# Kernel tuning notes

Measured on AMD Instinct MI355X. Metric: run time of the kernel, lower is better.

Reference implementation:

```python
import jax, jax.numpy as jnp
import numpy as np

N_NODES = 50000
N_EDGES = 262144
HID = 256
N_CLS = 2


def setup_inputs() -> dict:
    key = jax.random.key(0)
    ks = jax.random.split(key, 6)
    node_repr = jax.random.normal(ks[0], (N_NODES, HID), dtype=jnp.float32)
    src = jax.random.randint(ks[1], (N_EDGES,), 0, N_NODES, dtype=jnp.int64)
    dst = jax.random.randint(ks[2], (N_EDGES,), 0, N_NODES, dtype=jnp.int64)
    # Linear weights stored as (in, out); init ~ torch default scale
    W1 = jax.random.normal(ks[3], (4 * HID, 2 * HID), dtype=jnp.float32) * (1.0 / np.sqrt(4 * HID))
    b1 = jnp.zeros((2 * HID,), dtype=jnp.float32)
    W2 = jax.random.normal(ks[4], (2 * HID, N_CLS), dtype=jnp.float32) * (1.0 / np.sqrt(2 * HID))
    b2 = jnp.zeros((N_CLS,), dtype=jnp.float32)
    return {"node_repr": node_repr, "src": src, "dst": dst,
            "W1": W1, "b1": b1, "W2": W2, "b2": b2}


def reference(node_repr, src, dst, W1, b1, W2, b2):
    h_i = node_repr[src]                      # [E, H] gather
    h_j = node_repr[dst]                      # [E, H] gather
    edge_input = jnp.concatenate(
        [h_i, h_j, jnp.abs(h_i - h_j), h_i * h_j], axis=1)  # [E, 4H]
    h = jax.nn.relu(edge_input @ W1 + b1)     # [E, 2H]; dropout = identity (eval)
    return h @ W2 + b2                        # [E, C]
```

## Files before the change

kernel.cpp:

```cpp
#include <hip/hip_runtime.h>

#define N_NODES 50000
#define E_EDGES 262144

typedef __attribute__((ext_vector_type(8))) short bf16x8;
typedef __attribute__((ext_vector_type(4))) float f32x4;

union V16 { uint4 u; bf16x8 h; };

__device__ __forceinline__ unsigned rne_pack(float a, float b) {
  unsigned ua = __float_as_uint(a); ua += 0x7fffu + ((ua >> 16) & 1u);
  unsigned ub = __float_as_uint(b); ub += 0x7fffu + ((ub >> 16) & 1u);
  return (ua >> 16) | (ub & 0xffff0000u);
}
__device__ __forceinline__ float bflo(unsigned u) { return __uint_as_float(u << 16); }
__device__ __forceinline__ float bfhi(unsigned u) { return __uint_as_float(u & 0xffff0000u); }
__device__ __forceinline__ unsigned perm_pack(float a, float b) {
  return __builtin_amdgcn_perm(__float_as_uint(b), __float_as_uint(a), 0x07060302u);
}
__device__ __forceinline__ void async_gather16(const void* gptr, void* lptr) {
  __builtin_amdgcn_global_load_lds(
      (const __attribute__((address_space(1))) void*)gptr,
      (__attribute__((address_space(3))) void*)lptr, 16, 0, 0);
}

__global__ void cvt_node_kernel(const float* __restrict__ x, unsigned short* __restrict__ y) {
  int i = (blockIdx.x * 256 + threadIdx.x) * 8;
  float4 f0 = *(const float4*)(x + i);
  float4 f1 = *(const float4*)(x + i + 4);
  uint4 o;
  o.x = rne_pack(f0.x, f0.y);
  o.y = rne_pack(f0.z, f0.w);
  o.z = rne_pack(f1.x, f1.y);
  o.w = rne_pack(f1.z, f1.w);
  *(uint4*)(y + i) = o;
}

__global__ void prep_w1pp2_kernel(const float* __restrict__ w1, unsigned short* __restrict__ w1pp2) {
  int t = blockIdx.x * 256 + threadIdx.x;
  int step = t >> 13;
  int rem = t & 8191;
  int sq = rem >> 9;
  int col = rem & 511;
  int s = sq >> 2, qd = sq & 3;
  int k0 = s * 256 + step * 32 + qd * 8;
  float f[8];
#pragma unroll
  for (int i = 0; i < 8; ++i) f[i] = w1[(size_t)(k0 + i) * 512 + col];
  uint4 o;
  o.x = rne_pack(f[0], f[1]);
  o.y = rne_pack(f[2], f[3]);
  o.z = rne_pack(f[4], f[5]);
  o.w = rne_pack(f[6], f[7]);
  *(uint4*)(w1pp2 + (size_t)t * 8) = o;
}

__global__ void init_out_kernel(float* __restrict__ out, const float* __restrict__ b2) {
  int i = blockIdx.x * 256 + threadIdx.x;
  float2 v; v.x = b2[0]; v.y = b2[1];
  *(float2*)(out + (size_t)i * 2) = v;
}

__global__ __launch_bounds__(256, 2) void edge_mlp_kernel(
    const unsigned short* __restrict__ nodeb,
    const unsigned short* __restrict__ w1pp2,
    const int* __restrict__ src,
    const int* __restrict__ dst,
    const float* __restrict__ b1,
    const float* __restrict__ w2,
    float* __restrict__ out) {
  __shared__ char smem[65536];

  const int tid = threadIdx.x;
  const int wid = tid >> 6;
  const int lane = tid & 63;
  const int quad = lane >> 4;
  const int l16 = lane & 15;
  const int bx = blockIdx.x;
  const int xc = bx & 7;
  const int t2 = bx >> 3;
  const int n_idx = t2 & 7;
  const int m_idx = (t2 >> 3) * 8 + xc;
  const int row0 = m_idx * 256;
  const int wrow0 = row0 + wid * 64;
  const int n0 = n_idx * 64;

  const char* nodeB = (const char*)nodeb;
  const char* w1B = (const char*)w1pp2;

  unsigned oi[4], oj[4];
#pragma unroll
  for (int c = 0; c < 4; ++c) {
    int e = (wid * 4 + c) * 16 + (lane >> 2);
    unsigned qg = (unsigned)(((lane & 3) ^ ((lane >> 3) & 3)) << 4);
    oi[c] = ((unsigned)src[row0 + e] << 9) + qg;
    oj[c] = ((unsigned)dst[row0 + e] << 9) + qg;
  }
  unsigned bOff[4];
#pragma unroll
  for (int s = 0; s < 4; ++s)
    bOff[s] = (unsigned)((s * 4 + quad) * 8192 + (n0 + l16) * 16);
  const char* w1s = w1B;

  const unsigned aR = (unsigned)((wid * 64 + l16) * 64 + ((quad ^ ((l16 >> 1) & 3)) << 4));

  f32x4 acc[4][4];
#pragma unroll
  for (int mt = 0; mt < 4; ++mt)
#pragma unroll
    for (int nt = 0; nt < 4; ++nt)
      acc[mt][nt] = (f32x4){0.f, 0.f, 0.f, 0.f};

#pragma unroll
  for (int c = 0; c < 4; ++c) {
    async_gather16(nodeB + oi[c], smem + (wid * 4 + c) * 1024);
    async_gather16(nodeB + oj[c], smem + 16384 + (wid * 4 + c) * 1024);
  }
  __syncthreads();

  int p = 0;
#pragma unroll 1
  for (int step = 0; step < 8; ++step) {
    const char* Acur = smem + (p << 15);
    V16 bf[4][4];
#pragma unroll
    for (int s = 0; s < 4; ++s)
#pragma unroll
      for (int nt = 0; nt < 4; ++nt)
        bf[s][nt].u = *(const uint4*)(w1s + bOff[s] + nt * 256);
    if (step < 7) {
      const unsigned aoN = (unsigned)(step + 1) * 64u;
      char* Aalt = smem + ((p ^ 1) << 15);
#pragma unroll
      for (int c = 0; c < 4; ++c) {
        async_gather16(nodeB + (oi[c] + aoN), Aalt + (wid * 4 + c) * 1024);
        async_gather16(nodeB + (oj[c] + aoN), Aalt + 16384 + (wid * 4 + c) * 1024);
      }
    }
    V16 hi[4], hj[4];
#pragma unroll
    for (int mt = 0; mt < 4; ++mt) {
      hi[mt].u = *(const uint4*)(Acur + aR + mt * 1024);
      hj[mt].u = *(const uint4*)(Acur + 16384 + aR + mt * 1024);
    }
#pragma unroll
    for (int sl = 0; sl < 2; ++sl) {
#pragma unroll
      for (int mt = 0; mt < 4; ++mt) {
        bf16x8 af = (sl == 0) ? hi[mt].h : hj[mt].h;
#pragma unroll
        for (int nt = 0; nt < 4; ++nt)
          acc[mt][nt] = __builtin_amdgcn_mfma_f32_16x16x32_bf16(af, bf[sl][nt].h, acc[mt][nt], 0, 0, 0);
      }
    }
#pragma unroll
    for (int mt = 0; mt < 4; ++mt) {
      const unsigned hw[4] = {hi[mt].u.x, hi[mt].u.y, hi[mt].u.z, hi[mt].u.w};
      const unsigned jw[4] = {hj[mt].u.x, hj[mt].u.y, hj[mt].u.z, hj[mt].u.w};
      unsigned d[4], pr[4];
#pragma unroll
      for (int w = 0; w < 4; ++w) {
        float i0 = bflo(hw[w]), i1 = bfhi(hw[w]);
        float j0 = bflo(jw[w]), j1 = bfhi(jw[w]);
        d[w] = perm_pack(i0 - j0, i1 - j1) & 0x7fff7fffu;
        pr[w] = perm_pack(i0 * j0, i1 * j1);
      }
      V16 a2, a3;
      a2.u = make_uint4(d[0], d[1], d[2], d[3]);
      a3.u = make_uint4(pr[0], pr[1], pr[2], pr[3]);
#pragma unroll
      for (int nt = 0; nt < 4; ++nt)
        acc[mt][nt] = __builtin_amdgcn_mfma_f32_16x16x32_bf16(a2.h, bf[2][nt].h, acc[mt][nt], 0, 0, 0);
#pragma unroll
      for (int nt = 0; nt < 4; ++nt)
        acc[mt][nt] = __builtin_amdgcn_mfma_f32_16x16x32_bf16(a3.h, bf[3][nt].h, acc[mt][nt], 0, 0, 0);
    }
    __syncthreads();
    w1s += 131072;
    p ^= 1;
  }

#pragma unroll
  for (int mt = 0; mt < 4; ++mt) {
    float pc0[4] = {0.f, 0.f, 0.f, 0.f};
    float pc1[4] = {0.f, 0.f, 0.f, 0.f};
#pragma unroll
    for (int nt = 0; nt < 4; ++nt) {
      int gc = n0 + nt * 16 + l16;
      float b1v = b1[gc];
      float w20 = w2[gc * 2 + 0];
      float w21 = w2[gc * 2 + 1];
#pragma unroll
      for (int r = 0; r < 4; ++r) {
        float v = fmaxf(acc[mt][nt][r] + b1v, 0.f);
        pc0[r] = fmaf(v, w20, pc0[r]);
        pc1[r] = fmaf(v, w21, pc1[r]);
      }
    }
#pragma unroll
    for (int r = 0; r < 4; ++r) {
      float s0 = pc0[r], s1 = pc1[r];
#pragma unroll
      for (int off = 1; off < 16; off <<= 1) {
        s0 += __shfl_xor(s0, off);
        s1 += __shfl_xor(s1, off);
      }
      int e = wrow0 + mt * 16 + quad * 4 + r;
      if (l16 == 0) unsafeAtomicAdd(&out[(size_t)e * 2 + 0], s0);
      if (l16 == 1) unsafeAtomicAdd(&out[(size_t)e * 2 + 1], s1);
    }
  }
}

extern "C" void kernel_launch(void* const* d_in, const int* in_sizes, int n_in,
                              void* d_out, int out_size, void* d_ws, size_t ws_size,
                              hipStream_t stream) {
  const float* node = (const float*)d_in[0];
  const int* src = (const int*)d_in[1];
  const int* dst = (const int*)d_in[2];
  const float* W1 = (const float*)d_in[3];
  const float* b1 = (const float*)d_in[4];
  const float* W2 = (const float*)d_in[5];
  const float* b2 = (const float*)d_in[6];
  float* out = (float*)d_out;

  unsigned short* nodeb = (unsigned short*)d_ws;
  unsigned short* w1pp2 = (unsigned short*)((char*)d_ws + 25600000);

  cvt_node_kernel<<<6250, 256, 0, stream>>>(node, nodeb);
  prep_w1pp2_kernel<<<256, 256, 0, stream>>>(W1, w1pp2);
  init_out_kernel<<<1024, 256, 0, stream>>>(out, b2);
  edge_mlp_kernel<<<8192, 256, 0, stream>>>(nodeb, w1pp2, src, dst, b1, W2, out);
}
```

Measured before the change: 493.6 us.

## Retile edge MLP to 64-edge blocks with full-K gather staged once in LDS

Each block now covers 64 edges by 256 output columns, with the four waves splitting N instead of M. The full 256-wide bf16 rows for src and dst (64 KB) are gathered into LDS once with an XOR swizzle, so the per-step double-buffered gather and the per-step __syncthreads go away. The intent is to cut redundant node gathers, since fewer N-tiles now re-read the same edges, and to remove barrier stalls. In exchange each wave must stream more W1 columns per edge, and occupancy drops because 64 KB of LDS per block and the relaxed launch bounds allow fewer resident blocks.

```diff
diff --git a/kernel.cpp b/kernel.cpp
--- a/kernel.cpp
+++ b/kernel.cpp
@@ -61,7 +61,7 @@
   *(float2*)(out + (size_t)i * 2) = v;
 }
 
-__global__ __launch_bounds__(256, 2) void edge_mlp_kernel(
+__global__ __launch_bounds__(256) void edge_mlp_kernel(
     const unsigned short* __restrict__ nodeb,
     const unsigned short* __restrict__ w1pp2,
     const int* __restrict__ src,
@@ -79,30 +79,22 @@
   const int bx = blockIdx.x;
   const int xc = bx & 7;
   const int t2 = bx >> 3;
-  const int n_idx = t2 & 7;
-  const int m_idx = (t2 >> 3) * 8 + xc;
-  const int row0 = m_idx * 256;
-  const int wrow0 = row0 + wid * 64;
-  const int n0 = n_idx * 64;
+  const int n_half = t2 & 1;
+  const int m_idx = (t2 >> 1) * 8 + xc;
+  const int row0 = m_idx * 64;
+  const int n0 = n_half * 256 + wid * 64;
 
   const char* nodeB = (const char*)nodeb;
   const char* w1B = (const char*)w1pp2;
 
-  unsigned oi[4], oj[4];
-#pragma unroll
-  for (int c = 0; c < 4; ++c) {
-    int e = (wid * 4 + c) * 16 + (lane >> 2);
-    unsigned qg = (unsigned)(((lane & 3) ^ ((lane >> 3) & 3)) << 4);
-    oi[c] = ((unsigned)src[row0 + e] << 9) + qg;
-    oj[c] = ((unsigned)dst[row0 + e] << 9) + qg;
-  }
   unsigned bOff[4];
 #pragma unroll
   for (int s = 0; s < 4; ++s)
     bOff[s] = (unsigned)((s * 4 + quad) * 8192 + (n0 + l16) * 16);
   const char* w1s = w1B;
 
-  const unsigned aR = (unsigned)((wid * 64 + l16) * 64 + ((quad ^ ((l16 >> 1) & 3)) << 4));
+  const unsigned aXor = (unsigned)(l16 & 7);
+  const unsigned aBase = (unsigned)(l16 * 512);
 
   f32x4 acc[4][4];
 #pragma unroll
@@ -111,37 +103,35 @@
     for (int nt = 0; nt < 4; ++nt)
       acc[mt][nt] = (f32x4){0.f, 0.f, 0.f, 0.f};
 
-#pragma unroll
-  for (int c = 0; c < 4; ++c) {
-    async_gather16(nodeB + oi[c], smem + (wid * 4 + c) * 1024);
-    async_gather16(nodeB + oj[c], smem + 16384 + (wid * 4 + c) * 1024);
+  {
+    const int eh = tid >> 5;
+    const unsigned wsw = (unsigned)(((tid & 31) ^ (eh & 7)) << 4);
+#pragma unroll
+    for (int c = 0; c < 8; ++c) {
+      int e = c * 8 + eh;
+      unsigned so = ((unsigned)src[row0 + e] << 9) + wsw;
+      unsigned do_ = ((unsigned)dst[row0 + e] << 9) + wsw;
+      async_gather16(nodeB + so, smem + c * 4096 + wid * 1024);
+      async_gather16(nodeB + do_, smem + 32768 + c * 4096 + wid * 1024);
+    }
   }
   __syncthreads();
 
-  int p = 0;
-#pragma unroll 1
+#pragma unroll 2
   for (int step = 0; step < 8; ++step) {
-    const char* Acur = smem + (p << 15);
     V16 bf[4][4];
 #pragma unroll
     for (int s = 0; s < 4; ++s)
 #pragma unroll
       for (int nt = 0; nt < 4; ++nt)
         bf[s][nt].u = *(const uint4*)(w1s + bOff[s] + nt * 256);
-    if (step < 7) {
-      const unsigned aoN = (unsigned)(step + 1) * 64u;
-      char* Aalt = smem + ((p ^ 1) << 15);
-#pragma unroll
-      for (int c = 0; c < 4; ++c) {
-        async_gather16(nodeB + (oi[c] + aoN), Aalt + (wid * 4 + c) * 1024);
-        async_gather16(nodeB + (oj[c] + aoN), Aalt + 16384 + (wid * 4 + c) * 1024);
-      }
-    }
+    const unsigned stq = (unsigned)(step * 4 + quad);
     V16 hi[4], hj[4];
 #pragma unroll
     for (int mt = 0; mt < 4; ++mt) {
-      hi[mt].u = *(const uint4*)(Acur + aR + mt * 1024);
-      hj[mt].u = *(const uint4*)(Acur + 16384 + aR + mt * 1024);
+      unsigned ao = (unsigned)(mt * 16 * 512) + aBase + ((stq ^ aXor) << 4);
+      hi[mt].u = *(const uint4*)(smem + ao);
+      hj[mt].u = *(const uint4*)(smem + 32768 + ao);
     }
 #pragma unroll
     for (int sl = 0; sl < 2; ++sl) {
@@ -175,9 +165,7 @@
       for (int nt = 0; nt < 4; ++nt)
         acc[mt][nt] = __builtin_amdgcn_mfma_f32_16x16x32_bf16(a3.h, bf[3][nt].h, acc[mt][nt], 0, 0, 0);
     }
-    __syncthreads();
     w1s += 131072;
-    p ^= 1;
   }
 
 #pragma unroll
@@ -205,7 +193,7 @@
         s0 += __shfl_xor(s0, off);
         s1 += __shfl_xor(s1, off);
       }
-      int e = wrow0 + mt * 16 + quad * 4 + r;
+      int e = row0 + mt * 16 + quad * 4 + r;
       if (l16 == 0) unsafeAtomicAdd(&out[(size_t)e * 2 + 0], s0);
       if (l16 == 1) unsafeAtomicAdd(&out[(size_t)e * 2 + 1], s1);
     }
```

Result: faster. 411.7 us (-16.6%).
